# Performance work log

Hardware: AMD Instinct MI355X
Metric: run time of the kernel (lower is better)

Reference implementation:

```python
import jax, jax.numpy as jnp
import numpy as np

EPS = 1e-10
LN_EPS = 1e-5
WIN = 64          # entropy_window_size
STRIDE = WIN // 2 # 32
CDF_POINTS = 64   # entropy_cdf_points
D_MODEL = 256
STATS_DIM = 256 + 1 + CDF_POINTS  # 321
HID = 2 * D_MODEL  # 512


def setup_inputs() -> dict:
    key = jax.random.key(0)
    ks = jax.random.split(key, 8)
    B, L = 64, 65536
    x = jax.random.randint(ks[0], (B, L), 0, 256)

    def lin(k, fan_in, fan_out):
        return jax.random.normal(k, (fan_in, fan_out), jnp.float32) * (1.0 / np.sqrt(fan_in))

    return {
        "x": x,
        "W1": lin(ks[1], STATS_DIM, HID), "b1": jnp.zeros((HID,), jnp.float32),
        "g1": jnp.ones((HID,), jnp.float32), "be1": jnp.zeros((HID,), jnp.float32),
        "W2": lin(ks[2], HID, HID), "b2": jnp.zeros((HID,), jnp.float32),
        "g2": jnp.ones((HID,), jnp.float32), "be2": jnp.zeros((HID,), jnp.float32),
        "W3": lin(ks[3], HID, D_MODEL), "b3": jnp.zeros((D_MODEL,), jnp.float32),
    }


def _entropy(counts):
    # Shannon entropy (bits) over last axis; matches torch compute_entropy.
    total = counts.sum(axis=-1, keepdims=True)
    probs = counts / (total + EPS)
    return -(probs * jnp.log2(probs + EPS)).sum(axis=-1)


def _layernorm(h, g, b):
    mu = h.mean(axis=-1, keepdims=True)
    var = ((h - mu) ** 2).mean(axis=-1, keepdims=True)
    return (h - mu) * jax.lax.rsqrt(var + LN_EPS) * g + b


def reference(x, W1, b1, g1, be1, W2, b2, g2, be2, W3, b3):
    B, L = x.shape
    xb = jnp.clip(x, 0, 255)

    # Global byte histogram via scatter-add (no one-hot materialization).
    hist = jnp.zeros((B, 256), jnp.float32).at[jnp.arange(B)[:, None], xb].add(1.0)
    normalized_hist = hist / (jnp.float32(L) + EPS)
    global_entropy = _entropy(hist)[:, None]  # [B,1]

    nw = (L - WIN) // STRIDE + 1
    widx = jnp.arange(nw)[:, None] * STRIDE + jnp.arange(WIN)[None, :]
    wins = xb[:, widx].reshape(B * nw, WIN)
    rows = jnp.arange(B * nw)[:, None]
    whist = jnp.zeros((B * nw, 256), jnp.float32).at[rows, wins].add(1.0)
    went = _entropy(whist).reshape(B, nw)  # [B, nw]

    # Empirical CDF of window entropies at linspace(0,8,CDF_POINTS).
    levels = jnp.linspace(0.0, 8.0, CDF_POINTS)
    cdf = (went[:, :, None] <= levels[None, None, :]).astype(jnp.float32).mean(axis=1)

    feats = jnp.concatenate([normalized_hist, global_entropy, cdf], axis=1)  # [B, 321]

    # Projector MLP (dropout omitted: eval mode).
    h = _layernorm(feats @ W1 + b1, g1, be1)
    h = jax.nn.relu(h)
    h = _layernorm(h @ W2 + b2, g2, be2)
    h = jax.nn.relu(h)
    return h @ W3 + b3  # [B, d_model]
```

## Files before the change

### kernel.cpp

```cpp
#include <hip/hip_runtime.h>

#define BATCH 64
#define LLEN 65536
#define NW 2047
#define STATS 321
#define NCHUNK 32

__device__ __forceinline__ float dppWaveSumBcast(float x) {
    float t;
    t = __int_as_float(__builtin_amdgcn_update_dpp(0, __float_as_int(x), 0x111, 0xf, 0xf, true));  x += t;
    t = __int_as_float(__builtin_amdgcn_update_dpp(0, __float_as_int(x), 0x112, 0xf, 0xf, true));  x += t;
    t = __int_as_float(__builtin_amdgcn_update_dpp(0, __float_as_int(x), 0x114, 0xf, 0xf, true));  x += t;
    t = __int_as_float(__builtin_amdgcn_update_dpp(0, __float_as_int(x), 0x118, 0xf, 0xf, true));  x += t;
    t = __int_as_float(__builtin_amdgcn_update_dpp(0, __float_as_int(x), 0x142, 0xa, 0xf, false)); x += t;
    t = __int_as_float(__builtin_amdgcn_update_dpp(0, __float_as_int(x), 0x143, 0xc, 0xf, false)); x += t;
    return __int_as_float(__builtin_amdgcn_readlane(__float_as_int(x), 63));
}

__global__ __launch_bounds__(256) void front_kernel(const int* __restrict__ x,
                                                    int* __restrict__ hpart,
                                                    int* __restrict__ cpart) {
    __shared__ int lh[256];
    __shared__ int lc[256];
    const int row = blockIdx.y;
    const int c = blockIdx.x;
    const int t = threadIdx.x;
    lh[t] = 0;
    __syncthreads();

    const int base = row * LLEN + c * 2048;
#pragma unroll
    for (int it = 0; it < 8; ++it) {
        int v = x[base + it * 256 + t];
        atomicAdd(&lh[min(max(v, 0), 255)], 1);
    }

    const int lane = t & 63;
    const int wave = t >> 6;
    const float lv = (lane == 63) ? 8.0f : (float)lane * (8.0f / 63.0f);
    const float T = (6.0f - lv) * 64.0f;
    const int wbase = c * 64 + wave * 16;

    int vv[16];
#pragma unroll
    for (int i = 0; i < 16; ++i) {
        const int w = min(wbase + i, NW - 1);
        vv[i] = x[row * LLEN + (w << 5) + lane];
    }
    int cnt = 0;
#pragma unroll
    for (int i = 0; i < 16; ++i) {
        const int v = vv[i];
        unsigned long long m = ~0ull;
#pragma unroll
        for (int k = 0; k < 8; ++k) {
            const unsigned long long b = __ballot(v & (1 << k));
            m &= ((v >> k) & 1) ? b : ~b;
        }
        const float S = dppWaveSumBcast(__log2f((float)__popcll(m)));
        cnt += (int)((S >= T) && (wbase + i < NW));
    }
    lc[t] = cnt;
    __syncthreads();

    hpart[(row * NCHUNK + c) * 256 + t] = lh[t];
    if (t < 64)
        cpart[(row * NCHUNK + c) * 64 + t] = lc[t] + lc[64 + t] + lc[128 + t] + lc[192 + t];
}

__global__ __launch_bounds__(256) void gemm1_kernel(
    const int* __restrict__ hpart, const int* __restrict__ cpart,
    const float* __restrict__ W, const float* __restrict__ b,
    float* __restrict__ out) {
    __shared__ float sa[STATS];
    __shared__ float red[4];
    __shared__ float part[16][64];
    const int row = blockIdx.y;
    const int t = threadIdx.x;

    int h = 0;
    const int* hp = hpart + row * (NCHUNK * 256) + t;
#pragma unroll
    for (int ch = 0; ch < NCHUNK; ++ch) h += hp[ch * 256];
    const float p = (float)h * (1.0f / 65536.0f);
    sa[t] = p;
    const float term = -p * log2f(p + 1e-10f);
    const float s = dppWaveSumBcast(term);
    if ((t & 63) == 0) red[t >> 6] = s;

    if (t < 64) {
        int cc = 0;
        const int* cp = cpart + row * (NCHUNK * 64) + t;
#pragma unroll
        for (int ch = 0; ch < NCHUNK; ++ch) cc += cp[ch * 64];
        sa[257 + t] = (float)cc * (1.0f / 2047.0f);
    }
    __syncthreads();
    if (t == 0) sa[256] = red[0] + red[1] + red[2] + red[3];
    __syncthreads();

    const int cl = (t & 15) * 4;
    const int col = blockIdx.x * 64 + cl;
    const int kg = t >> 4;
    const int klo = kg * 21;
    const int khi = min(klo + 21, STATS);
    float4 acc = {0.f, 0.f, 0.f, 0.f};
    for (int k = klo; k < khi; ++k) {
        const float a = sa[k];
        const float4 w = *(const float4*)&W[k * 512 + col];
        acc.x = fmaf(a, w.x, acc.x);
        acc.y = fmaf(a, w.y, acc.y);
        acc.z = fmaf(a, w.z, acc.z);
        acc.w = fmaf(a, w.w, acc.w);
    }
    *(float4*)&part[kg][cl] = acc;
    __syncthreads();
    if (t < 64) {
        float o = b[blockIdx.x * 64 + t];
#pragma unroll
        for (int g = 0; g < 16; ++g) o += part[g][t];
        out[row * 512 + blockIdx.x * 64 + t] = o;
    }
}

template <int NOUT, int CPB>
__global__ __launch_bounds__(256) void gemm_ln_kernel(
    const float* __restrict__ raw, const float* __restrict__ g,
    const float* __restrict__ be, const float* __restrict__ W,
    const float* __restrict__ b, float* __restrict__ out) {
    constexpr int TC = CPB / 4;
    constexpr int KG = 256 / TC;
    constexpr int KI = 512 / KG;
    __shared__ float sa[512];
    __shared__ float red[8];
    __shared__ float part[KG][CPB];
    const int row = blockIdx.y;
    const int t = threadIdx.x;

    const float v1 = raw[row * 512 + t];
    const float v2 = raw[row * 512 + 256 + t];
    const float s = dppWaveSumBcast(v1 + v2);
    const float q = dppWaveSumBcast(v1 * v1 + v2 * v2);
    if ((t & 63) == 0) { red[t >> 6] = s; red[4 + (t >> 6)] = q; }
    __syncthreads();
    const float mu = (red[0] + red[1] + red[2] + red[3]) * (1.0f / 512.0f);
    const float var = (red[4] + red[5] + red[6] + red[7]) * (1.0f / 512.0f) - mu * mu;
    const float rs = rsqrtf(var + 1e-5f);
    sa[t] = fmaxf((v1 - mu) * rs * g[t] + be[t], 0.0f);
    sa[t + 256] = fmaxf((v2 - mu) * rs * g[t + 256] + be[t + 256], 0.0f);
    __syncthreads();

    const int cl = (t % TC) * 4;
    const int col = blockIdx.x * CPB + cl;
    const int kg = t / TC;
    float4 acc = {0.f, 0.f, 0.f, 0.f};
#pragma unroll
    for (int i = 0; i < KI; ++i) {
        const int k = kg * KI + i;
        const float a = sa[k];
        const float4 w = *(const float4*)&W[k * NOUT + col];
        acc.x = fmaf(a, w.x, acc.x);
        acc.y = fmaf(a, w.y, acc.y);
        acc.z = fmaf(a, w.z, acc.z);
        acc.w = fmaf(a, w.w, acc.w);
    }
    *(float4*)&part[kg][cl] = acc;
    __syncthreads();
    if (t < CPB) {
        float o = b[blockIdx.x * CPB + t];
#pragma unroll
        for (int gi = 0; gi < KG; ++gi) o += part[gi][t];
        out[row * NOUT + blockIdx.x * CPB + t] = o;
    }
}

extern "C" void kernel_launch(void* const* d_in, const int* in_sizes, int n_in,
                              void* d_out, int out_size, void* d_ws, size_t ws_size,
                              hipStream_t stream) {
    const int* x = (const int*)d_in[0];
    const float* W1 = (const float*)d_in[1];
    const float* b1 = (const float*)d_in[2];
    const float* g1 = (const float*)d_in[3];
    const float* be1 = (const float*)d_in[4];
    const float* W2 = (const float*)d_in[5];
    const float* b2 = (const float*)d_in[6];
    const float* g2 = (const float*)d_in[7];
    const float* be2 = (const float*)d_in[8];
    const float* W3 = (const float*)d_in[9];
    const float* b3 = (const float*)d_in[10];
    float* out = (float*)d_out;

    char* ws = (char*)d_ws;
    int* hpart = (int*)ws;
    int* cpart = (int*)(ws + 2097152);
    float* raw1 = (float*)(ws + 2621440);
    float* raw2 = (float*)(ws + 2752512);

    front_kernel<<<dim3(NCHUNK, BATCH), 256, 0, stream>>>(x, hpart, cpart);
    gemm1_kernel<<<dim3(8, BATCH), 256, 0, stream>>>(hpart, cpart, W1, b1, raw1);
    gemm_ln_kernel<512, 64><<<dim3(8, BATCH), 256, 0, stream>>>(raw1, g1, be1, W2, b2, raw2);
    gemm_ln_kernel<256, 32><<<dim3(8, BATCH), 256, 0, stream>>>(raw2, g2, be2, W3, b3, out);
}
```

Before: 120.8 us.

## Reuse ballot bitmasks across overlapping windows and fold histogram into match masks

The front kernel now loads each wave's 512 contiguous bytes once, plus a 64-byte halo, instead of separate histogram loads and per-window loads. It computes 8 bit-plane ballots per 64-byte block and reuses them for both the aligned window and the half-offset overlapping window, roughly halving ballot work. The global histogram is built from the same match masks: the first lane of each value group adds the group count with one atomic, which replaces per-element LDS atomics. This adds register pressure from the two ballot mask arrays and a cross-half shuffle per window.

```diff
diff --git a/kernel.cpp b/kernel.cpp
--- a/kernel.cpp
+++ b/kernel.cpp
@@ -25,40 +25,76 @@
     const int row = blockIdx.y;
     const int c = blockIdx.x;
     const int t = threadIdx.x;
-    lh[t] = 0;
-    __syncthreads();
-
-    const int base = row * LLEN + c * 2048;
-#pragma unroll
-    for (int it = 0; it < 8; ++it) {
-        int v = x[base + it * 256 + t];
-        atomicAdd(&lh[min(max(v, 0), 255)], 1);
-    }
-
     const int lane = t & 63;
     const int wave = t >> 6;
+    lh[t] = 0;
+    __syncthreads();
+
+    const int* xr = x + row * LLEN;
+    const int eb = c * 2048 + wave * 512;
+
+    int e[9];
+#pragma unroll
+    for (int j = 0; j < 8; ++j) e[j] = min(max(xr[eb + j * 64 + lane], 0), 255);
+    e[8] = min(max(xr[min(eb + 512, LLEN - 64) + lane], 0), 255);
+
     const float lv = (lane == 63) ? 8.0f : (float)lane * (8.0f / 63.0f);
     const float T = (6.0f - lv) * 64.0f;
     const int wbase = c * 64 + wave * 16;
-
-    int vv[16];
-#pragma unroll
-    for (int i = 0; i < 16; ++i) {
-        const int w = min(wbase + i, NW - 1);
-        vv[i] = x[row * LLEN + (w << 5) + lane];
-    }
+    const int xlane = lane ^ 32;
+
+    unsigned Blo[8], Bhi[8];
+#pragma unroll
+    for (int k = 0; k < 8; ++k) {
+        const unsigned long long b = __ballot(e[0] & (1 << k));
+        Blo[k] = (unsigned)b;
+        Bhi[k] = (unsigned)(b >> 32);
+    }
+
     int cnt = 0;
 #pragma unroll
-    for (int i = 0; i < 16; ++i) {
-        const int v = vv[i];
-        unsigned long long m = ~0ull;
+    for (int j = 0; j < 8; ++j) {
+        unsigned Nlo[8], Nhi[8];
 #pragma unroll
         for (int k = 0; k < 8; ++k) {
-            const unsigned long long b = __ballot(v & (1 << k));
-            m &= ((v >> k) & 1) ? b : ~b;
+            const unsigned long long b = __ballot(e[j + 1] & (1 << k));
+            Nlo[k] = (unsigned)b;
+            Nhi[k] = (unsigned)(b >> 32);
         }
-        const float S = dppWaveSumBcast(__log2f((float)__popcll(m)));
-        cnt += (int)((S >= T) && (wbase + i < NW));
+        const int srcv = (lane < 32) ? e[j + 1] : e[j];
+        const int u = __shfl(srcv, xlane);
+
+        {
+            unsigned mlo = 0xffffffffu, mhi = 0xffffffffu;
+#pragma unroll
+            for (int k = 0; k < 8; ++k) {
+                const unsigned s = (unsigned)(((e[j] >> k) & 1) - 1);
+                mlo &= Blo[k] ^ s;
+                mhi &= Bhi[k] ^ s;
+            }
+            const int cc = __popc(mlo) + __popc(mhi);
+            const float S = dppWaveSumBcast(__log2f((float)cc));
+            cnt += (int)(S >= T);
+            unsigned below = __builtin_amdgcn_mbcnt_lo(mlo, 0u);
+            below = __builtin_amdgcn_mbcnt_hi(mhi, below);
+            if (below == 0u) atomicAdd(&lh[e[j]], cc);
+        }
+
+        {
+            unsigned mlo = 0xffffffffu, mhi = 0xffffffffu;
+#pragma unroll
+            for (int k = 0; k < 8; ++k) {
+                const unsigned s = (unsigned)(((u >> k) & 1) - 1);
+                mlo &= Bhi[k] ^ s;
+                mhi &= Nlo[k] ^ s;
+            }
+            const int cc = __popc(mlo) + __popc(mhi);
+            const float S = dppWaveSumBcast(__log2f((float)cc));
+            cnt += (int)((S >= T) && (wbase + 2 * j + 1 < NW));
+        }
+
+#pragma unroll
+        for (int k = 0; k < 8; ++k) { Blo[k] = Nlo[k]; Bhi[k] = Nhi[k]; }
     }
     lc[t] = cnt;
     __syncthreads();
```

Result: faster. 113.1 us (-6.4%).
